# Kernel optimization log

Measured on AMD Instinct MI355X. Metric: run time of the kernel, lower is better.

The kernel has to match this reference:

```python
import jax, jax.numpy as jnp
import numpy as np

WINDOW = 15          # window_size from __init__
EPS = 1e-8           # torch cosine_similarity eps


def setup_inputs() -> dict:
    B, S, D, NSPK = 4, 4096, 128, 9
    key = jax.random.key(0)
    k1, k2, k3 = jax.random.split(key, 3)
    x = jax.random.normal(k1, (B, S, D), dtype=jnp.float32)
    qmask = jax.random.uniform(k2, (S, B, NSPK), dtype=jnp.float32)
    # realistic dialogue lengths: between S//2 and S
    dia_len = jax.random.randint(k3, (B,), S // 2, S + 1, dtype=jnp.int32)
    return {"x": x, "qmask": qmask, "dia_len": dia_len}


def reference(x, qmask, dia_len):
    # x: [B,S,D], qmask: [S,B,NSPK], dia_len: [B]
    B, S, _ = x.shape
    xs = jax.lax.stop_gradient(x)  # original detaches x before similarity
    norms = jnp.maximum(jnp.linalg.norm(xs, axis=-1, keepdims=True), EPS)
    xn = xs / norms
    # cosine similarity, clamped, mapped to angular weight in [0,1]
    cos = jnp.clip(jnp.einsum('bid,bjd->bij', xn, xn), -1.0, 1.0)
    w = 1.0 - jnp.arccos(cos) / jnp.pi                       # [B,S,S]

    idx = jnp.arange(S)
    win = jnp.abs(idx[:, None] - idx[None, :]) <= WINDOW     # [S,S]
    valid = idx[None, :] < dia_len[:, None]                  # [B,S]
    M = win[None, :, :] & valid[:, :, None] & valid[:, None, :]  # [B,S,S]

    speakers = jnp.argmax(qmask, axis=-1).T                  # [B,S]
    same = speakers[:, :, None] == speakers[:, None, :]      # [B,S,S]

    # count of same-speaker tokens inside window (includes i itself);
    # doubling applied only when count > 1
    cnt = jnp.sum(M & same, axis=-1)                         # [B,S]
    dbl = (cnt > 1)[:, :, None] & same                       # [B,S,S]

    adj = w * M.astype(w.dtype) * (1.0 + dbl.astype(w.dtype))

    # symmetric-ish degree normalization D^-1/2 A D^-1/2 (row-sum degrees)
    deg = adj.sum(axis=-1)
    deg = jnp.where(deg == 0, 1.0, deg)
    dinv = deg ** -0.5
    adj = dinv[:, :, None] * adj * dinv[:, None, :]
    return adj
```

## Files before the change

### kernel.cpp

```cpp
#include <hip/hip_runtime.h>
#include <math.h>

#define BB 4
#define SS 4096
#define DD 128
#define NSPK 9
#define WIN 15
#define BANDW 31
#define EPSN 1e-8f
#define INV_PI 0.31830988618379067f

__global__ __launch_bounds__(256) void k_prep(const float* __restrict__ x,
                                              const float* __restrict__ qmask,
                                              float* __restrict__ xn,
                                              int* __restrict__ spk) {
    int wid  = (blockIdx.x * blockDim.x + threadIdx.x) >> 6;
    int lane = threadIdx.x & 63;
    if (wid >= BB * SS) return;

    const float2* xr = (const float2*)(x + (size_t)wid * DD);
    float2 v = xr[lane];
    float ss = v.x * v.x + v.y * v.y;
    #pragma unroll
    for (int off = 32; off; off >>= 1) ss += __shfl_xor(ss, off);
    float inv = 1.0f / fmaxf(sqrtf(ss), EPSN);
    float2 o; o.x = v.x * inv; o.y = v.y * inv;
    ((float2*)(xn + (size_t)wid * DD))[lane] = o;

    if (lane == 0) {
        int b = wid / SS, s = wid % SS;
        const float* q = qmask + ((size_t)s * BB + b) * NSPK;
        float best = q[0]; int bi = 0;
        #pragma unroll
        for (int k = 1; k < NSPK; ++k) {
            float qv = q[k];
            if (qv > best) { best = qv; bi = k; }
        }
        spk[wid] = bi;
    }
}

__global__ __launch_bounds__(256) void k_band(const float* __restrict__ xn,
                                              const int* __restrict__ spk,
                                              const int* __restrict__ dia_len,
                                              float* __restrict__ band,
                                              float* __restrict__ dinv) {
    int row  = (blockIdx.x * blockDim.x + threadIdx.x) >> 6;
    int lane = threadIdx.x & 63;
    if (row >= BB * SS) return;
    int b = row / SS, i = row % SS;
    int len = dia_len[b];
    int j = i - WIN + lane;
    bool inr   = (lane < BANDW) && (j >= 0) && (j < SS);
    bool maskv = inr && (i < len) && (j < len);

    bool same = false;
    if (inr) same = (spk[row] == spk[b * SS + j]);

    float aij = 0.f;
    if (maskv) {
        const float4* xi = (const float4*)(xn + (size_t)row * DD);
        const float4* xj = (const float4*)(xn + ((size_t)b * SS + j) * DD);
        float d0 = 0.f, d1 = 0.f;
        #pragma unroll
        for (int d = 0; d < DD / 8; ++d) {
            float4 a0 = xi[2 * d],     c0 = xj[2 * d];
            float4 a1 = xi[2 * d + 1], c1 = xj[2 * d + 1];
            d0 += a0.x * c0.x + a0.y * c0.y + a0.z * c0.z + a0.w * c0.w;
            d1 += a1.x * c1.x + a1.y * c1.y + a1.z * c1.z + a1.w * c1.w;
        }
        float dot = d0 + d1;
        dot = fminf(fmaxf(dot, -1.f), 1.f);
        aij = 1.f - acosf(dot) * INV_PI;
    }

    unsigned long long bal = __ballot(maskv && same);
    int cnt = __popcll(bal);
    if (maskv && same && cnt > 1) aij *= 2.f;

    float deg = aij;
    #pragma unroll
    for (int off = 32; off; off >>= 1) deg += __shfl_xor(deg, off);

    if (lane < 32) band[(size_t)row * 32 + lane] = aij;
    if (lane == 0) {
        float dv = (deg == 0.f) ? 1.f : deg;
        dinv[row] = 1.0f / sqrtf(dv);
    }
}

__global__ __launch_bounds__(256) void k_write(const float* __restrict__ band,
                                               const float* __restrict__ dinv,
                                               float* __restrict__ out) {
    int t = blockIdx.x * blockDim.x + threadIdx.x;
    int row = t >> 5, l = t & 31;
    if (row >= BB * SS) return;
    int b = row / SS, i = row % SS;
    int j = i - WIN + l;
    if (l < BANDW && j >= 0 && j < SS) {
        float v = band[(size_t)row * 32 + l] * dinv[row] * dinv[b * SS + j];
        out[(size_t)row * SS + j] = v;
    }
}

extern "C" void kernel_launch(void* const* d_in, const int* in_sizes, int n_in,
                              void* d_out, int out_size, void* d_ws, size_t ws_size,
                              hipStream_t stream) {
    const float* x       = (const float*)d_in[0];
    const float* qmask   = (const float*)d_in[1];
    const int*   dia_len = (const int*)d_in[2];
    float* out = (float*)d_out;

    char* ws = (char*)d_ws;
    const size_t rows = (size_t)BB * SS;
    float* xn   = (float*)ws;
    int*   spk  = (int*)  (ws + rows * DD * 4);
    float* dinv = (float*)(ws + rows * DD * 4 + rows * 4);
    float* band = (float*)(ws + rows * DD * 4 + 2 * rows * 4);

    hipMemsetAsync(d_out, 0, (size_t)out_size * sizeof(float), stream);

    int nrows = BB * SS;
    k_prep <<<nrows / 4, 256, 0, stream>>>(x, qmask, xn, spk);
    k_band <<<nrows / 4, 256, 0, stream>>>(xn, spk, dia_len, band, dinv);
    k_write<<<nrows * 32 / 256, 256, 0, stream>>>(band, dinv, out);
}
```

Before: 306.7 us.

## Fuse normalization, speaker argmax and zero-fill into band kernel; drop memset

Merges the prep and band kernels so each wave handles two rows in its halves. Norms and speaker ids are computed on the fly from raw x and qmask instead of going through a workspace round trip. The full-output memset is replaced by nontemporal vector zero stores that skip the band region, and the final kernel writes whole aligned float4 spans around the band. This cuts one kernel launch and the extra pass over the 256 MB output, at the cost of recomputing each neighbour's norm and argmax per band entry.

```diff
diff --git a/kernel.cpp b/kernel.cpp
--- a/kernel.cpp
+++ b/kernel.cpp
@@ -6,101 +6,124 @@
 #define DD 128
 #define NSPK 9
 #define WIN 15
-#define BANDW 31
 #define EPSN 1e-8f
 #define INV_PI 0.31830988618379067f
 
-__global__ __launch_bounds__(256) void k_prep(const float* __restrict__ x,
+typedef float vfloat4 __attribute__((ext_vector_type(4)));
+
+__global__ __launch_bounds__(256) void k_main(const float* __restrict__ x,
                                               const float* __restrict__ qmask,
-                                              float* __restrict__ xn,
-                                              int* __restrict__ spk) {
+                                              const int* __restrict__ dia_len,
+                                              float* __restrict__ band,
+                                              float* __restrict__ dinv,
+                                              float* __restrict__ out) {
     int wid  = (blockIdx.x * blockDim.x + threadIdx.x) >> 6;
     int lane = threadIdx.x & 63;
-    if (wid >= BB * SS) return;
+    int half = lane >> 5;
+    int hl   = lane & 31;
 
-    const float2* xr = (const float2*)(x + (size_t)wid * DD);
-    float2 v = xr[lane];
-    float ss = v.x * v.x + v.y * v.y;
-    #pragma unroll
-    for (int off = 32; off; off >>= 1) ss += __shfl_xor(ss, off);
-    float inv = 1.0f / fmaxf(sqrtf(ss), EPSN);
-    float2 o; o.x = v.x * inv; o.y = v.y * inv;
-    ((float2*)(xn + (size_t)wid * DD))[lane] = o;
+    int row = wid * 2 + half;
+    int b   = row >> 12;
+    int i   = row & (SS - 1);
+    int len = dia_len[b];
 
-    if (lane == 0) {
-        int b = wid / SS, s = wid % SS;
-        const float* q = qmask + ((size_t)s * BB + b) * NSPK;
-        float best = q[0]; int bi = 0;
+    int  j     = i - WIN + hl;
+    bool inr   = (hl < 31) && (j >= 0) && (j < SS);
+    bool maskv = inr && (i < len) && (j < len);
+
+    int sj = 0;
+    if (inr) {
+        const float* q = qmask + ((size_t)j * BB + b) * NSPK;
+        float best = q[0];
         #pragma unroll
         for (int k = 1; k < NSPK; ++k) {
             float qv = q[k];
-            if (qv > best) { best = qv; bi = k; }
+            if (qv > best) { best = qv; sj = k; }
         }
-        spk[wid] = bi;
     }
-}
+    int si = __shfl(sj, (lane & 32) + WIN);
+    bool same = inr && (sj == si);
 
-__global__ __launch_bounds__(256) void k_band(const float* __restrict__ xn,
-                                              const int* __restrict__ spk,
-                                              const int* __restrict__ dia_len,
-                                              float* __restrict__ band,
-                                              float* __restrict__ dinv) {
-    int row  = (blockIdx.x * blockDim.x + threadIdx.x) >> 6;
-    int lane = threadIdx.x & 63;
-    if (row >= BB * SS) return;
-    int b = row / SS, i = row % SS;
-    int len = dia_len[b];
-    int j = i - WIN + lane;
-    bool inr   = (lane < BANDW) && (j >= 0) && (j < SS);
-    bool maskv = inr && (i < len) && (j < len);
-
-    bool same = false;
-    if (inr) same = (spk[row] == spk[b * SS + j]);
-
-    float aij = 0.f;
+    float dot = 0.f, nj2 = 0.f;
     if (maskv) {
-        const float4* xi = (const float4*)(xn + (size_t)row * DD);
-        const float4* xj = (const float4*)(xn + ((size_t)b * SS + j) * DD);
-        float d0 = 0.f, d1 = 0.f;
+        const float4* xi = (const float4*)(x + (size_t)row * DD);
+        const float4* xj = (const float4*)(x + ((size_t)b * SS + j) * DD);
+        float d0 = 0.f, d1 = 0.f, n0 = 0.f, n1 = 0.f;
         #pragma unroll
         for (int d = 0; d < DD / 8; ++d) {
             float4 a0 = xi[2 * d],     c0 = xj[2 * d];
             float4 a1 = xi[2 * d + 1], c1 = xj[2 * d + 1];
             d0 += a0.x * c0.x + a0.y * c0.y + a0.z * c0.z + a0.w * c0.w;
             d1 += a1.x * c1.x + a1.y * c1.y + a1.z * c1.z + a1.w * c1.w;
+            n0 += c0.x * c0.x + c0.y * c0.y + c0.z * c0.z + c0.w * c0.w;
+            n1 += c1.x * c1.x + c1.y * c1.y + c1.z * c1.z + c1.w * c1.w;
         }
-        float dot = d0 + d1;
-        dot = fminf(fmaxf(dot, -1.f), 1.f);
-        aij = 1.f - acosf(dot) * INV_PI;
+        dot = d0 + d1;
+        nj2 = n0 + n1;
+    }
+    float ni2 = __shfl(nj2, (lane & 32) + WIN);
+
+    float aij = 0.f;
+    if (maskv) {
+        float ni = fmaxf(sqrtf(ni2), EPSN);
+        float nj = fmaxf(sqrtf(nj2), EPSN);
+        float c  = dot / (ni * nj);
+        c = fminf(fmaxf(c, -1.f), 1.f);
+        aij = 1.f - acosf(c) * INV_PI;
     }
 
     unsigned long long bal = __ballot(maskv && same);
-    int cnt = __popcll(bal);
+    unsigned long long hm  = half ? 0xFFFFFFFF00000000ull : 0x00000000FFFFFFFFull;
+    int cnt = __popcll(bal & hm);
     if (maskv && same && cnt > 1) aij *= 2.f;
 
     float deg = aij;
     #pragma unroll
-    for (int off = 32; off; off >>= 1) deg += __shfl_xor(deg, off);
+    for (int off = 16; off; off >>= 1) deg += __shfl_xor(deg, off);
 
-    if (lane < 32) band[(size_t)row * 32 + lane] = aij;
-    if (lane == 0) {
+    band[(size_t)row * 32 + hl] = aij;
+    if (hl == 0) {
         float dv = (deg == 0.f) ? 1.f : deg;
         dinv[row] = 1.0f / sqrtf(dv);
     }
+
+    int rA = wid * 2, iA = rA & (SS - 1);
+    int rB = rA + 1,  iB = rB & (SS - 1);
+    int fsA = (iA - WIN < 0 ? 0 : iA - WIN) >> 2;
+    int feA = (iA + WIN > SS - 1 ? SS - 1 : iA + WIN) >> 2;
+    int fsB = (iB - WIN < 0 ? 0 : iB - WIN) >> 2;
+    int feB = (iB + WIN > SS - 1 ? SS - 1 : iB + WIN) >> 2;
+
+    vfloat4 z = (vfloat4)(0.f);
+    vfloat4* oA = (vfloat4*)(out + (size_t)rA * SS);
+    vfloat4* oB = (vfloat4*)(out + (size_t)rB * SS);
+    #pragma unroll
+    for (int it = 0; it < SS / 4 / 64; ++it) {
+        int f = it * 64 + lane;
+        if (f < fsA || f > feA) __builtin_nontemporal_store(z, oA + f);
+        if (f < fsB || f > feB) __builtin_nontemporal_store(z, oB + f);
+    }
 }
 
-__global__ __launch_bounds__(256) void k_write(const float* __restrict__ band,
-                                               const float* __restrict__ dinv,
-                                               float* __restrict__ out) {
-    int t = blockIdx.x * blockDim.x + threadIdx.x;
-    int row = t >> 5, l = t & 31;
+__global__ __launch_bounds__(256) void k_bw(const float* __restrict__ band,
+                                            const float* __restrict__ dinv,
+                                            float* __restrict__ out) {
+    int row  = (blockIdx.x * blockDim.x + threadIdx.x) >> 6;
+    int lane = threadIdx.x & 63;
     if (row >= BB * SS) return;
-    int b = row / SS, i = row % SS;
-    int j = i - WIN + l;
-    if (l < BANDW && j >= 0 && j < SS) {
-        float v = band[(size_t)row * 32 + l] * dinv[row] * dinv[b * SS + j];
-        out[(size_t)row * SS + j] = v;
+    int b = row >> 12, i = row & (SS - 1);
+    int j0 = i - WIN; if (j0 < 0) j0 = 0;
+    int j1 = i + WIN; if (j1 > SS - 1) j1 = SS - 1;
+    int fs = j0 >> 2, fe = j1 >> 2;
+
+    int j = fs * 4 + lane;
+    if (j > fe * 4 + 3) return;
+
+    float v = 0.f;
+    if (j >= j0 && j <= j1) {
+        v = band[(size_t)row * 32 + (j - i + WIN)] * dinv[row] * dinv[b * SS + j];
     }
+    __builtin_nontemporal_store(v, out + (size_t)row * SS + j);
 }
 
 extern "C" void kernel_launch(void* const* d_in, const int* in_sizes, int n_in,
@@ -113,15 +136,10 @@
 
     char* ws = (char*)d_ws;
     const size_t rows = (size_t)BB * SS;
-    float* xn   = (float*)ws;
-    int*   spk  = (int*)  (ws + rows * DD * 4);
-    float* dinv = (float*)(ws + rows * DD * 4 + rows * 4);
-    float* band = (float*)(ws + rows * DD * 4 + 2 * rows * 4);
+    float* band = (float*)ws;
+    float* dinv = (float*)(ws + rows * 32 * 4);
 
-    hipMemsetAsync(d_out, 0, (size_t)out_size * sizeof(float), stream);
-
-    int nrows = BB * SS;
-    k_prep <<<nrows / 4, 256, 0, stream>>>(x, qmask, xn, spk);
-    k_band <<<nrows / 4, 256, 0, stream>>>(xn, spk, dia_len, band, dinv);
-    k_write<<<nrows * 32 / 256, 256, 0, stream>>>(band, dinv, out);
+    k_main<<<(int)(rows / 2 * 64 / 256), 256, 0, stream>>>(x, qmask, dia_len,
+                                                           band, dinv, out);
+    k_bw  <<<(int)(rows * 64 / 256),     256, 0, stream>>>(band, dinv, out);
 }
```

Result: faster. 288.5 us (-5.9%).
